# Optimization experiments

Hardware: AMD Instinct MI355X
Metric: run time of the kernel (lower is better)

Reference implementation:

```python
import jax, jax.numpy as jnp
import numpy as np

N = 50000
E = 1600000


def _gcn_norm(edge_index, num_nodes):
    # PyG gcn_norm with add_self_loops=True, edge_weight=1:
    # append self loops, deg = in-degree over dst (col), norm = d_src^-1/2 * d_dst^-1/2
    loops = jnp.arange(num_nodes, dtype=edge_index.dtype)
    src = jnp.concatenate([edge_index[0], loops])
    dst = jnp.concatenate([edge_index[1], loops])
    deg = jax.ops.segment_sum(jnp.ones_like(dst, dtype=jnp.float32), dst,
                              num_segments=num_nodes)
    dinv = jnp.where(deg > 0, jax.lax.rsqrt(deg), 0.0)
    norm = dinv[src] * dinv[dst]  # [E+N]
    return src, dst, norm


def _gcn_layer(x, W, b, src, dst, norm, num_nodes):
    h = x @ W                                  # [N, out]
    msg = h[src] * norm[:, None]               # gather + scale, [E+N, out]
    out = jax.ops.segment_sum(msg, dst, num_segments=num_nodes)
    return out + b


def setup_inputs() -> dict:
    key = jax.random.key(0)
    ks = jax.random.split(key, 10)
    d_in, d_h, d_out = 128, 128, 64
    s = lambda d: 1.0 / np.sqrt(d)
    return {
        "x": jax.random.normal(ks[0], (N, d_in), dtype=jnp.float32),
        "edge_index": jax.random.randint(ks[1], (2, E), 0, N, dtype=jnp.int64),
        "W1": jax.random.normal(ks[2], (d_in, d_h), dtype=jnp.float32) * s(d_in),
        "b1": jnp.zeros((d_h,), dtype=jnp.float32),
        "W2": jax.random.normal(ks[3], (d_h, d_h), dtype=jnp.float32) * s(d_h),
        "b2": jnp.zeros((d_h,), dtype=jnp.float32),
        "W3": jax.random.normal(ks[4], (d_h, d_h), dtype=jnp.float32) * s(d_h),
        "b3": jnp.zeros((d_h,), dtype=jnp.float32),
        "W4": jax.random.normal(ks[5], (d_h, d_out), dtype=jnp.float32) * s(d_h),
        "b4": jnp.zeros((d_out,), dtype=jnp.float32),
    }


def reference(x, edge_index, W1, b1, W2, b2, W3, b3, W4, b4):
    src, dst, norm = _gcn_norm(edge_index, N)
    h = jax.nn.relu(_gcn_layer(x, W1, b1, src, dst, norm, N))
    h = jax.nn.relu(_gcn_layer(h, W2, b2, src, dst, norm, N))
    h = jax.nn.relu(_gcn_layer(h, W3, b3, src, dst, norm, N))
    h = _gcn_layer(h, W4, b4, src, dst, norm, N)
    return h
```

## Files before the change

kernel.cpp:

```cpp
#include <hip/hip_runtime.h>
#include <hip/hip_fp16.h>

constexpr int K_DIM = 128;

typedef _Float16 f16x8 __attribute__((ext_vector_type(8)));
typedef float f32x4 __attribute__((ext_vector_type(4)));

#define GLOAD16(g, l) __builtin_amdgcn_global_load_lds( \
    (const __attribute__((address_space(1))) void*)(g), \
    (__attribute__((address_space(3))) void*)(l), 16, 0, 0)

__global__ void zerob_k(int* __restrict__ bcount, int NBr) {
  int t = threadIdx.x;
  if (t < NBr) bcount[t] = 0;
}

__global__ __launch_bounds__(256) void bcount_k(const int* __restrict__ dst, int E,
    int* __restrict__ bcount, int NBr) {
  __shared__ int h[256];
  const int tid = threadIdx.x;
  h[tid] = 0;
  __syncthreads();
  for (int t = blockIdx.x * 256 + tid; t < E; t += gridDim.x * 256)
    atomicAdd(&h[dst[t] >> 8], 1);
  __syncthreads();
  if (tid < NBr && h[tid]) atomicAdd(&bcount[tid], h[tid]);
}

__global__ __launch_bounds__(256) void bscan_k(const int* __restrict__ bcount,
    int* __restrict__ bstart, int* __restrict__ bcursor, int NBr) {
  __shared__ int sh[256];
  const int t = threadIdx.x;
  sh[t] = (t < NBr) ? bcount[t] : 0;
  __syncthreads();
  for (int off = 1; off < 256; off <<= 1) {
    int w = (t >= off) ? sh[t - off] : 0;
    __syncthreads();
    sh[t] += w;
    __syncthreads();
  }
  if (t < NBr) {
    int ex = t ? sh[t - 1] : 0;
    bstart[t] = ex;
    bcursor[t] = ex;
  }
  if (t == NBr - 1) bstart[NBr] = sh[t];
}

__global__ __launch_bounds__(256) void bscatter_k(const int* __restrict__ ei, int E,
    int* __restrict__ bcursor, unsigned* __restrict__ brec, int NBr) {
  __shared__ int h[256];
  __shared__ int base[256];
  const int tid = threadIdx.x;
  h[tid] = 0;
  __syncthreads();
  const int chunk = (E + gridDim.x - 1) / gridDim.x;
  const int s = blockIdx.x * chunk;
  const int e = min(E, s + chunk);
  for (int t = s + tid; t < e; t += 256) atomicAdd(&h[ei[E + t] >> 8], 1);
  __syncthreads();
  if (tid < NBr && h[tid]) base[tid] = atomicAdd(&bcursor[tid], h[tid]);
  __syncthreads();
  for (int t = s + tid; t < e; t += 256) {
    int src = ei[t];
    int d = ei[E + t];
    int bk = d >> 8;
    int p = atomicAdd(&base[bk], 1);
    brec[p] = ((unsigned)src << 8) | (unsigned)(d & 255);
  }
}

__global__ __launch_bounds__(256) void bcsr_k(const unsigned* __restrict__ brec,
    const int* __restrict__ bstart, int n, int E,
    int* __restrict__ rowptr, int* __restrict__ colidx, float* __restrict__ dinv) {
  __shared__ int s_deg[256];
  __shared__ int s_cur[256];
  __shared__ int s_lrp[257];
  const int b = blockIdx.x, tid = threadIdx.x;
  const int node0 = b << 8;
  const int LC = min(256, n - node0);
  const int rs = bstart[b], cnt = bstart[b + 1] - rs;

  s_deg[tid] = (tid < LC) ? 1 : 0;
  __syncthreads();
  for (int i = tid; i < cnt; i += 256) atomicAdd(&s_deg[brec[rs + i] & 255], 1);
  __syncthreads();
  s_cur[tid] = s_deg[tid];
  __syncthreads();
  for (int off = 1; off < 256; off <<= 1) {
    int w = (tid >= off) ? s_cur[tid - off] : 0;
    __syncthreads();
    s_cur[tid] += w;
    __syncthreads();
  }
  s_lrp[tid + 1] = s_cur[tid];
  if (tid == 0) s_lrp[0] = 0;
  __syncthreads();

  const int gbase = rs + node0;
  if (tid < LC) {
    int p = s_lrp[tid];
    colidx[gbase + p] = node0 + tid;
    s_cur[tid] = p + 1;
    rowptr[node0 + tid] = gbase + p;
    dinv[node0 + tid] = rsqrtf((float)(s_lrp[tid + 1] - p));
  }
  __syncthreads();
  for (int i = tid; i < cnt; i += 256) {
    unsigned r = brec[rs + i];
    int p = atomicAdd(&s_cur[r & 255], 1);
    colidx[gbase + p] = (int)(r >> 8);
  }
  if (b == (int)gridDim.x - 1 && tid == 0) rowptr[n] = E + n;
}

__global__ __launch_bounds__(256) void split_k(const float* __restrict__ x,
    __half* __restrict__ z, long total4) {
  long t = (long)blockIdx.x * 256 + threadIdx.x;
  if (t >= total4) return;
  float4 v = reinterpret_cast<const float4*>(x)[t];
  union { __half2 h[2]; uint2 u; } uu;
  uu.h[0] = __floats2half2_rn(v.x, v.y);
  uu.h[1] = __floats2half2_rn(v.z, v.w);
  reinterpret_cast<uint2*>(z)[t] = uu.u;
}

__global__ __launch_bounds__(256) void wprep_k(
    const float* __restrict__ W1, const float* __restrict__ W2,
    const float* __restrict__ W3, const float* __restrict__ W4,
    __half* __restrict__ wth, __half* __restrict__ wtl) {
  int id = blockIdx.x * 256 + threadIdx.x;
  if (id >= 57344) return;
  const float* W;
  int nout, base, rem;
  if (id < 49152) {
    int l = id / 16384;
    W = (l == 0) ? W1 : (l == 1) ? W2 : W3;
    nout = 128;
    base = l * 16384;
    rem = id - base;
  } else {
    W = W4;
    nout = 64;
    base = 49152;
    rem = id - base;
  }
  int k = rem / nout, c = rem % nout;
  float w = W[k * nout + c];
  __half hi = __float2half_rn(w);
  __half lo = __float2half_rn(w - __half2float(hi));
  wth[base + c * 128 + k] = hi;
  wtl[base + c * 128 + k] = lo;
}

template<int NOUT>
__global__ __launch_bounds__(256) void gemm_mfma_k(
    const __half* __restrict__ Z,
    const __half* __restrict__ Wh, const __half* __restrict__ Wl,
    const float* __restrict__ dinv, __half* __restrict__ H, int n) {
  constexpr int NT = NOUT / 16;
  __shared__ __half Az[64][32];
  __shared__ __half Bh[NOUT][32];
  __shared__ __half Bl[NOUT][32];
  const int tid = threadIdx.x;
  const int lane = tid & 63;
  const int w = tid >> 6;
  const int r16 = lane & 15;
  const int kb = lane >> 4;
  const int row0 = blockIdx.x * 64;
  const int sw = (r16 + (r16 >> 2)) & 3;

  f32x4 acc[NT];
  #pragma unroll
  for (int t = 0; t < NT; ++t)
    #pragma unroll
    for (int q = 0; q < 4; ++q) acc[t][q] = 0.f;

  char* AzB = (char*)&Az[0][0];
  char* BhB = (char*)&Bh[0][0];
  char* BlB = (char*)&Bl[0][0];

  for (int kc = 0; kc < 128; kc += 32) {
    __syncthreads();
    {
      int r = tid >> 2;
      int q = (tid & 3) ^ ((r + (r >> 2)) & 3);
      int rc = row0 + r; rc = (rc < n) ? rc : (n - 1);
      GLOAD16(Z + (size_t)rc * 128 + kc + q * 8, AzB + w * 1024);
    }
    {
      int c = tid >> 2;
      int q = (tid & 3) ^ ((c + (c >> 2)) & 3);
      GLOAD16(Wh + (size_t)c * 128 + kc + q * 8, BhB + w * 1024);
      GLOAD16(Wl + (size_t)c * 128 + kc + q * 8, BlB + w * 1024);
      if constexpr (NOUT == 128) {
        int i1 = tid + 256;
        int c1 = i1 >> 2;
        int q1 = (i1 & 3) ^ ((c1 + (c1 >> 2)) & 3);
        GLOAD16(Wh + (size_t)c1 * 128 + kc + q1 * 8, BhB + 4096 + w * 1024);
        GLOAD16(Wl + (size_t)c1 * 128 + kc + q1 * 8, BlB + 4096 + w * 1024);
      }
    }
    __syncthreads();

    const int ao = (kb ^ sw) * 8;
    f16x8 az = *(const f16x8*)&Az[w * 16 + r16][ao];
    #pragma unroll
    for (int t = 0; t < NT; ++t) {
      f16x8 bh = *(const f16x8*)&Bh[t * 16 + r16][ao];
      f16x8 bl = *(const f16x8*)&Bl[t * 16 + r16][ao];
      acc[t] = __builtin_amdgcn_mfma_f32_16x16x32_f16(az, bh, acc[t], 0, 0, 0);
      acc[t] = __builtin_amdgcn_mfma_f32_16x16x32_f16(az, bl, acc[t], 0, 0, 0);
    }
  }

  #pragma unroll
  for (int q = 0; q < 4; ++q) {
    int grow = row0 + w * 16 + kb * 4 + q;
    if (grow < n) {
      float dsc = dinv[grow];
      #pragma unroll
      for (int t = 0; t < NT; ++t)
        H[(size_t)grow * NOUT + t * 16 + r16] = __float2half(dsc * acc[t][q]);
    }
  }
}

__global__ __launch_bounds__(256) void agg128_k(const __half* __restrict__ H,
    const int* __restrict__ rowptr, const int* __restrict__ colidx,
    const float* __restrict__ dinv, const float* __restrict__ bias,
    __half* __restrict__ Z, int n) {
  const int wave = threadIdx.x >> 6;
  const int lane = threadIdx.x & 63;
  const int node = blockIdx.x * 4 + wave;
  if (node >= n) return;
  const int s = rowptr[node], e = rowptr[node + 1];
  const __half2* H2 = reinterpret_cast<const __half2*>(H);

  float ax = 0.f, ay = 0.f;
  for (int base = s; base < e; base += 64) {
    int m = e - base;
    int c = __builtin_nontemporal_load(&colidx[base + ((lane < m) ? lane : 0)]);
    int kmax = (m < 64) ? m : 64;
    int k = 0;
    for (; k + 7 < kmax; k += 8) {
      int cc[8];
      float2 hh[8];
      #pragma unroll
      for (int u = 0; u < 8; ++u) cc[u] = __shfl(c, k + u);
      #pragma unroll
      for (int u = 0; u < 8; ++u) hh[u] = __half22float2(H2[(size_t)cc[u] * 64 + lane]);
      #pragma unroll
      for (int u = 0; u < 8; ++u) { ax += hh[u].x; ay += hh[u].y; }
    }
    for (; k < kmax; ++k) {
      int ck = __shfl(c, k);
      float2 h = __half22float2(H2[(size_t)ck * 64 + lane]);
      ax += h.x;
      ay += h.y;
    }
  }
  float d = dinv[node];
  float2 b2 = reinterpret_cast<const float2*>(bias)[lane];
  float ox = fmaxf(fmaf(d, ax, b2.x), 0.f);
  float oy = fmaxf(fmaf(d, ay, b2.y), 0.f);
  __half2 hv = __floats2half2_rn(ox, oy);
  unsigned vv = *reinterpret_cast<unsigned*>(&hv);
  __builtin_nontemporal_store(vv, reinterpret_cast<unsigned*>(Z) + (size_t)node * 64 + lane);
}

__global__ __launch_bounds__(256) void agg64_k(const __half* __restrict__ H,
    const int* __restrict__ rowptr, const int* __restrict__ colidx,
    const float* __restrict__ dinv, const float* __restrict__ bias,
    float* __restrict__ out, int n) {
  const int wave = threadIdx.x >> 6;
  const int lane = threadIdx.x & 63;
  const int node = blockIdx.x * 4 + wave;
  if (node >= n) return;
  const int s = rowptr[node], e = rowptr[node + 1];

  float a0 = 0.f;
  for (int base = s; base < e; base += 64) {
    int m = e - base;
    int c = __builtin_nontemporal_load(&colidx[base + ((lane < m) ? lane : 0)]);
    int kmax = (m < 64) ? m : 64;
    int k = 0;
    for (; k + 7 < kmax; k += 8) {
      int cc[8];
      float hh[8];
      #pragma unroll
      for (int u = 0; u < 8; ++u) cc[u] = __shfl(c, k + u);
      #pragma unroll
      for (int u = 0; u < 8; ++u) hh[u] = __half2float(H[(size_t)cc[u] * 64 + lane]);
      #pragma unroll
      for (int u = 0; u < 8; ++u) a0 += hh[u];
    }
    for (; k < kmax; ++k) {
      int ck = __shfl(c, k);
      a0 += __half2float(H[(size_t)ck * 64 + lane]);
    }
  }
  float o = fmaf(dinv[node], a0, bias[lane]);
  __builtin_nontemporal_store(o, &out[(size_t)node * 64 + lane]);
}

extern "C" void kernel_launch(void* const* d_in, const int* in_sizes, int n_in,
                              void* d_out, int out_size, void* d_ws, size_t ws_size,
                              hipStream_t stream) {
  const int n = in_sizes[0] / K_DIM;
  const int E = in_sizes[1] / 2;
  const int NBr = (n + 255) >> 8;

  const float* x  = (const float*)d_in[0];
  const int*   ei = (const int*)d_in[1];
  const float* W1 = (const float*)d_in[2];
  const float* b1 = (const float*)d_in[3];
  const float* W2 = (const float*)d_in[4];
  const float* b2 = (const float*)d_in[5];
  const float* W3 = (const float*)d_in[6];
  const float* b3 = (const float*)d_in[7];
  const float* W4 = (const float*)d_in[8];
  const float* b4 = (const float*)d_in[9];
  float* out = (float*)d_out;

  char* ws = (char*)d_ws;
  size_t off = 0;
  auto alloc = [&](size_t bytes) -> void* {
    void* p = ws + off;
    off += (bytes + 255) & ~(size_t)255;
    return p;
  };
  int*      bcount  = (int*)     alloc(256 * 4);
  int*      bstart  = (int*)     alloc(257 * 4);
  int*      bcursor = (int*)     alloc(256 * 4);
  unsigned* brec    = (unsigned*)alloc((size_t)E * 4);
  int*      rowptr  = (int*)     alloc((size_t)(n + 1) * 4);
  int*      colidx  = (int*)     alloc((size_t)(E + n) * 4);
  float*    dinv    = (float*)   alloc((size_t)n * 4);
  __half*   Z       = (__half*)  alloc((size_t)n * 128 * 2);
  __half*   hH      = (__half*)  alloc((size_t)n * 128 * 2);
  __half*   wth     = (__half*)  alloc((size_t)57344 * 2);
  __half*   wtl     = (__half*)  alloc((size_t)57344 * 2);

  zerob_k<<<1, 256, 0, stream>>>(bcount, NBr);
  bcount_k<<<512, 256, 0, stream>>>(ei + E, E, bcount, NBr);
  bscan_k<<<1, 256, 0, stream>>>(bcount, bstart, bcursor, NBr);
  bscatter_k<<<256, 256, 0, stream>>>(ei, E, bcursor, brec, NBr);
  bcsr_k<<<NBr, 256, 0, stream>>>(brec, bstart, n, E, rowptr, colidx, dinv);

  const long total4 = (long)n * 32;
  split_k<<<(int)((total4 + 255) / 256), 256, 0, stream>>>(x, Z, total4);
  wprep_k<<<224, 256, 0, stream>>>(W1, W2, W3, W4, wth, wtl);

  const int gb = (n + 63) / 64;
  const int ab = (n + 3) / 4;

  gemm_mfma_k<128><<<gb, 256, 0, stream>>>(Z, wth, wtl, dinv, hH, n);
  agg128_k<<<ab, 256, 0, stream>>>(hH, rowptr, colidx, dinv, b1, Z, n);
  gemm_mfma_k<128><<<gb, 256, 0, stream>>>(Z, wth + 16384, wtl + 16384, dinv, hH, n);
  agg128_k<<<ab, 256, 0, stream>>>(hH, rowptr, colidx, dinv, b2, Z, n);
  gemm_mfma_k<128><<<gb, 256, 0, stream>>>(Z, wth + 32768, wtl + 32768, dinv, hH, n);
  agg128_k<<<ab, 256, 0, stream>>>(hH, rowptr, colidx, dinv, b3, Z, n);
  gemm_mfma_k<64><<<gb, 256, 0, stream>>>(Z, wth + 49152, wtl + 49152, dinv, hH, n);
  agg64_k<<<ab, 256, 0, stream>>>(hH, rowptr, colidx, dinv, b4, out, n);
}
```

Baseline: 316.8 us.

## Halve GEMM row tile to 32 with 2x2 wave split, fuse prep kernels

The MFMA GEMM now uses 32-row blocks, with the four waves arranged as 2 row halves by 2 column halves instead of four row strips. This doubles the number of blocks (more parallelism for N=50000) and halves the accumulators per wave, at the cost of loading the weight tile twice as often per row processed. The x-to-fp16 split and weight preparation kernels are merged into one launch. The bucket-count zeroing kernel is replaced by hipMemsetAsync.

Result: no change. 319.3 us (+0.8%).

```diff
diff --git a/kernel.cpp b/kernel.cpp
--- a/kernel.cpp
+++ b/kernel.cpp
@@ -9,11 +9,6 @@
 #define GLOAD16(g, l) __builtin_amdgcn_global_load_lds( \
     (const __attribute__((address_space(1))) void*)(g), \
     (__attribute__((address_space(3))) void*)(l), 16, 0, 0)
-
-__global__ void zerob_k(int* __restrict__ bcount, int NBr) {
-  int t = threadIdx.x;
-  if (t < NBr) bcount[t] = 0;
-}
 
 __global__ __launch_bounds__(256) void bcount_k(const int* __restrict__ dst, int E,
     int* __restrict__ bcount, int NBr) {
@@ -114,43 +109,42 @@
   if (b == (int)gridDim.x - 1 && tid == 0) rowptr[n] = E + n;
 }
 
-__global__ __launch_bounds__(256) void split_k(const float* __restrict__ x,
-    __half* __restrict__ z, long total4) {
-  long t = (long)blockIdx.x * 256 + threadIdx.x;
-  if (t >= total4) return;
-  float4 v = reinterpret_cast<const float4*>(x)[t];
-  union { __half2 h[2]; uint2 u; } uu;
-  uu.h[0] = __floats2half2_rn(v.x, v.y);
-  uu.h[1] = __floats2half2_rn(v.z, v.w);
-  reinterpret_cast<uint2*>(z)[t] = uu.u;
-}
-
-__global__ __launch_bounds__(256) void wprep_k(
+__global__ __launch_bounds__(256) void prep_k(const float* __restrict__ x,
+    __half* __restrict__ z, long total4,
     const float* __restrict__ W1, const float* __restrict__ W2,
     const float* __restrict__ W3, const float* __restrict__ W4,
     __half* __restrict__ wth, __half* __restrict__ wtl) {
-  int id = blockIdx.x * 256 + threadIdx.x;
-  if (id >= 57344) return;
-  const float* W;
-  int nout, base, rem;
-  if (id < 49152) {
-    int l = id / 16384;
-    W = (l == 0) ? W1 : (l == 1) ? W2 : W3;
-    nout = 128;
-    base = l * 16384;
-    rem = id - base;
-  } else {
-    W = W4;
-    nout = 64;
-    base = 49152;
-    rem = id - base;
-  }
-  int k = rem / nout, c = rem % nout;
-  float w = W[k * nout + c];
-  __half hi = __float2half_rn(w);
-  __half lo = __float2half_rn(w - __half2float(hi));
-  wth[base + c * 128 + k] = hi;
-  wtl[base + c * 128 + k] = lo;
+  long t = (long)blockIdx.x * 256 + threadIdx.x;
+  if (t < total4) {
+    float4 v = reinterpret_cast<const float4*>(x)[t];
+    union { __half2 h[2]; uint2 u; } uu;
+    uu.h[0] = __floats2half2_rn(v.x, v.y);
+    uu.h[1] = __floats2half2_rn(v.z, v.w);
+    reinterpret_cast<uint2*>(z)[t] = uu.u;
+  }
+  if (t < 57344) {
+    int id = (int)t;
+    const float* W;
+    int nout, base, rem;
+    if (id < 49152) {
+      int l = id / 16384;
+      W = (l == 0) ? W1 : (l == 1) ? W2 : W3;
+      nout = 128;
+      base = l * 16384;
+      rem = id - base;
+    } else {
+      W = W4;
+      nout = 64;
+      base = 49152;
+      rem = id - base;
+    }
+    int k = rem / nout, c = rem % nout;
+    float w = W[k * nout + c];
+    __half hi = __float2half_rn(w);
+    __half lo = __float2half_rn(w - __half2float(hi));
+    wth[base + c * 128 + k] = hi;
+    wtl[base + c * 128 + k] = lo;
+  }
 }
 
 template<int NOUT>
@@ -158,8 +152,8 @@
     const __half* __restrict__ Z,
     const __half* __restrict__ Wh, const __half* __restrict__ Wl,
     const float* __restrict__ dinv, __half* __restrict__ H, int n) {
-  constexpr int NT = NOUT / 16;
-  __shared__ __half Az[64][32];
+  constexpr int NT = NOUT / 32;
+  __shared__ __half Az[32][32];
   __shared__ __half Bh[NOUT][32];
   __shared__ __half Bl[NOUT][32];
   const int tid = threadIdx.x;
@@ -167,7 +161,9 @@
   const int w = tid >> 6;
   const int r16 = lane & 15;
   const int kb = lane >> 4;
-  const int row0 = blockIdx.x * 64;
+  const int row0 = blockIdx.x * 32;
+  const int rh = w & 1;
+  const int ch = w >> 1;
   const int sw = (r16 + (r16 >> 2)) & 3;
 
   f32x4 acc[NT];
@@ -182,7 +178,7 @@
 
   for (int kc = 0; kc < 128; kc += 32) {
     __syncthreads();
-    {
+    if (w < 2) {
       int r = tid >> 2;
       int q = (tid & 3) ^ ((r + (r >> 2)) & 3);
       int rc = row0 + r; rc = (rc < n) ? rc : (n - 1);
@@ -204,11 +200,12 @@
     __syncthreads();
 
     const int ao = (kb ^ sw) * 8;
-    f16x8 az = *(const f16x8*)&Az[w * 16 + r16][ao];
+    f16x8 az = *(const f16x8*)&Az[rh * 16 + r16][ao];
     #pragma unroll
     for (int t = 0; t < NT; ++t) {
-      f16x8 bh = *(const f16x8*)&Bh[t * 16 + r16][ao];
-      f16x8 bl = *(const f16x8*)&Bl[t * 16 + r16][ao];
+      int c = ch * (NOUT / 2) + t * 16 + r16;
+      f16x8 bh = *(const f16x8*)&Bh[c][ao];
+      f16x8 bl = *(const f16x8*)&Bl[c][ao];
       acc[t] = __builtin_amdgcn_mfma_f32_16x16x32_f16(az, bh, acc[t], 0, 0, 0);
       acc[t] = __builtin_amdgcn_mfma_f32_16x16x32_f16(az, bl, acc[t], 0, 0, 0);
     }
@@ -216,12 +213,14 @@
 
   #pragma unroll
   for (int q = 0; q < 4; ++q) {
-    int grow = row0 + w * 16 + kb * 4 + q;
+    int grow = row0 + rh * 16 + kb * 4 + q;
     if (grow < n) {
       float dsc = dinv[grow];
       #pragma unroll
-      for (int t = 0; t < NT; ++t)
-        H[(size_t)grow * NOUT + t * 16 + r16] = __float2half(dsc * acc[t][q]);
+      for (int t = 0; t < NT; ++t) {
+        int col = ch * (NOUT / 2) + t * 16 + r16;
+        H[(size_t)grow * NOUT + col] = __float2half(dsc * acc[t][q]);
+      }
     }
   }
 }
@@ -342,17 +341,17 @@
   __half*   wth     = (__half*)  alloc((size_t)57344 * 2);
   __half*   wtl     = (__half*)  alloc((size_t)57344 * 2);
 
-  zerob_k<<<1, 256, 0, stream>>>(bcount, NBr);
+  hipMemsetAsync(bcount, 0, 256 * 4, stream);
   bcount_k<<<512, 256, 0, stream>>>(ei + E, E, bcount, NBr);
   bscan_k<<<1, 256, 0, stream>>>(bcount, bstart, bcursor, NBr);
   bscatter_k<<<256, 256, 0, stream>>>(ei, E, bcursor, brec, NBr);
   bcsr_k<<<NBr, 256, 0, stream>>>(brec, bstart, n, E, rowptr, colidx, dinv);
 
   const long total4 = (long)n * 32;
-  split_k<<<(int)((total4 + 255) / 256), 256, 0, stream>>>(x, Z, total4);
-  wprep_k<<<224, 256, 0, stream>>>(W1, W2, W3, W4, wth, wtl);
-
-  const int gb = (n + 63) / 64;
+  prep_k<<<(int)((total4 + 255) / 256), 256, 0, stream>>>(x, Z, total4,
+                                                          W1, W2, W3, W4, wth, wtl);
+
+  const int gb = (n + 31) / 32;
   const int ab = (n + 3) / 4;
 
   gemm_mfma_k<128><<<gb, 256, 0, stream>>>(Z, wth, wtl, dinv, hH, n);
```
